# Optimization experiments

Measured on AMD Instinct MI355X. Metric: run time of the kernel, lower is better.

The kernel has to match this reference:

```python
import jax, jax.numpy as jnp
import numpy as np

DIM = 256
HEADS = 8
SEQ = 4096
SCALE = DIM ** -0.5  # note: original scales by full dim, not head dim


def setup_inputs() -> dict:
    key = jax.random.key(0)
    ks = jax.random.split(key, 5)
    x = jax.random.normal(ks[0], (SEQ, DIM), dtype=jnp.float32)
    w_qkv = jax.random.normal(ks[1], (DIM, 3 * DIM), dtype=jnp.float32) * (DIM ** -0.5)
    b_qkv = jnp.zeros((3 * DIM,), dtype=jnp.float32)
    w_out = jax.random.normal(ks[2], (DIM, DIM), dtype=jnp.float32) * (DIM ** -0.5)
    b_out = jnp.zeros((DIM,), dtype=jnp.float32)
    return {"x": x, "w_qkv": w_qkv, "b_qkv": b_qkv, "w_out": w_out, "b_out": b_out}


def reference(x, w_qkv, b_qkv, w_out, b_out):
    n, dim = x.shape
    h = HEADS
    d = dim // h
    qkv = x @ w_qkv + b_qkv                      # [n, 3*dim]
    q, k, v = jnp.split(qkv, 3, axis=-1)         # each [n, dim]
    # 'n (h d) -> h n d'
    q = q.reshape(n, h, d).transpose(1, 0, 2)
    k = k.reshape(n, h, d).transpose(1, 0, 2)
    v = v.reshape(n, h, d).transpose(1, 0, 2)
    dots = jnp.einsum('hid,hjd->hij', q, k) * SCALE  # [h, n, n]
    attn = jax.nn.softmax(dots, axis=-1)
    out = jnp.einsum('hij,hjd->hid', attn, v)        # [h, n, d]
    out = out.transpose(1, 0, 2).reshape(n, dim)     # 'h n d -> n (h d)'
    return out @ w_out + b_out                       # [n, dim]
```

## Files before the change

### kernel.cpp

```cpp
#include <hip/hip_runtime.h>
#include <stdint.h>

#define SEQ   4096
#define DIM   256
#define HDIM  32
#define HEADS 8
#define W3    768
#define LOG2E 1.4426950408889634f

typedef float  f32x4  __attribute__((ext_vector_type(4)));
typedef float  fl4    __attribute__((ext_vector_type(4)));
typedef short  bf16x8 __attribute__((ext_vector_type(8)));
typedef short  bf16x4 __attribute__((ext_vector_type(4)));

static __device__ __forceinline__ f32x4 MFMA_PV(bf16x4 a, bf16x4 b, f32x4 c) {
#if defined(__HIP_DEVICE_COMPILE__)
# if __has_builtin(__builtin_amdgcn_mfma_f32_16x16x16_bf16)
    return __builtin_amdgcn_mfma_f32_16x16x16_bf16(a, b, c, 0, 0, 0);
# elif __has_builtin(__builtin_amdgcn_mfma_f32_16x16x16bf16_1k)
    return __builtin_amdgcn_mfma_f32_16x16x16bf16_1k(a, b, c, 0, 0, 0);
# else
    f32x4 d;
    asm volatile("v_mfma_f32_16x16x16_bf16 %0, %1, %2, %3"
                 : "=v"(d) : "v"(a), "v"(b), "v"(c));
    return d;
# endif
#else
    (void)a; (void)b;
    return c;
#endif
}

__device__ __forceinline__ unsigned short f2bf(float f) {
    union { __bf16 h; unsigned short u; } v;
    v.h = (__bf16)f;
    return v.u;
}
__device__ __forceinline__ short f2bf_s(float f) {
    union { __bf16 h; short s; } v;
    v.h = (__bf16)f;
    return v.s;
}

__global__ __launch_bounds__(256) void prep_kernel(
    const float* __restrict__ x, const float* __restrict__ wqkv,
    const float* __restrict__ wout,
    unsigned short* __restrict__ xb,
    unsigned short* __restrict__ wt,
    unsigned short* __restrict__ wot)
{
    __shared__ float lds[64][65];
    const int b   = blockIdx.x;
    const int tid = threadIdx.x;
    if (b < 64) {
        const float* src;
        unsigned short* dst;
        int N, i0, j0;
        if (b < 48) {
            src = wqkv; dst = wt; N = W3;
            i0 = (b & 3) * 64; j0 = (b >> 2) * 64;
        } else {
            int bb = b - 48;
            src = wout; dst = wot; N = DIM;
            i0 = (bb & 3) * 64; j0 = (bb >> 2) * 64;
        }
        const int c = tid & 63, grp = tid >> 6;
        #pragma unroll
        for (int k = 0; k < 16; ++k) {
            int r = grp * 16 + k;
            lds[r][c] = src[(size_t)(i0 + r) * N + j0 + c];
        }
        __syncthreads();
        #pragma unroll
        for (int k = 0; k < 16; ++k) {
            int cc = grp * 16 + k;
            dst[(size_t)(j0 + cc) * DIM + i0 + c] = f2bf(lds[c][cc]);
        }
    } else {
        const fl4* __restrict__ x4 = (const fl4*)x;
        const int total4 = SEQ * DIM / 4;
        for (int i = (b - 64) * 256 + tid; i < total4; i += 64 * 256) {
            fl4 v = x4[i];
            ushort4 o;
            o.x = f2bf(v[0]); o.y = f2bf(v[1]);
            o.z = f2bf(v[2]); o.w = f2bf(v[3]);
            *reinterpret_cast<ushort4*>(xb + (size_t)i * 4) = o;
        }
    }
}

__global__ __launch_bounds__(256) void qkv_gemm(
    const unsigned short* __restrict__ xb,
    const unsigned short* __restrict__ wt,
    const float* __restrict__ bqkv,
    unsigned short* __restrict__ Qb,
    unsigned short* __restrict__ Kb,
    unsigned short* __restrict__ Vb)
{
    const int wid  = threadIdx.x >> 6;
    const int lane = threadIdx.x & 63;
    const int g    = lane >> 4, li = lane & 15;
    const int row0 = blockIdx.x * 64 + wid * 16;
    const int col0 = blockIdx.y * 64;

    f32x4 acc[4];
    #pragma unroll
    for (int c = 0; c < 4; ++c)
        acc[c] = (f32x4){0.f, 0.f, 0.f, 0.f};

    #pragma unroll
    for (int ks = 0; ks < DIM; ks += 32) {
        bf16x8 a = *(const bf16x8*)(xb + (size_t)(row0 + li) * DIM + ks + g * 8);
        bf16x8 b[4];
        #pragma unroll
        for (int c = 0; c < 4; ++c)
            b[c] = *(const bf16x8*)(wt + (size_t)(col0 + 16 * c + li) * DIM + ks + g * 8);
        #pragma unroll
        for (int c = 0; c < 4; ++c)
            acc[c] = __builtin_amdgcn_mfma_f32_16x16x32_bf16(a, b[c], acc[c], 0, 0, 0);
    }

    #pragma unroll
    for (int c = 0; c < 4; ++c)
        #pragma unroll
        for (int r = 0; r < 4; ++r) {
            int row = row0 + g * 4 + r;
            int col = col0 + 16 * c + li;
            float v = acc[c][r] + bqkv[col];
            int sec = col >> 8;
            int cc  = col & 255;
            int hh  = cc >> 5, dd = cc & 31;
            if (sec == 0)
                Qb[((size_t)hh * SEQ + row) * HDIM + dd] = f2bf(v * (0.0625f * LOG2E));
            else if (sec == 1)
                Kb[((size_t)hh * SEQ + row) * HDIM + dd] = f2bf(v);
            else
                Vb[(size_t)hh * SEQ * HDIM + ((size_t)(row >> 4) * HDIM + dd) * 16 + (row & 15)] = f2bf(v);
        }
}

__global__ __launch_bounds__(256) void attn_kernel(
    const unsigned short* __restrict__ Qb,
    const unsigned short* __restrict__ Kb,
    const unsigned short* __restrict__ Vb,
    float* __restrict__ Opart,
    float* __restrict__ Lp,
    int nc)
{
    const int wid  = threadIdx.x >> 6;
    const int lane = threadIdx.x & 63;
    const int g    = lane >> 4, li = lane & 15;
    const int head = blockIdx.y;
    const int chunk = blockIdx.z;
    const int r0   = blockIdx.x * 128 + wid * 32;
    const int span = SEQ / nc;
    const int jb0  = chunk * span;
    const int ntile = span / 64;

    const unsigned short* Qh = Qb + (size_t)head * SEQ * HDIM;
    const unsigned short* kp = Kb + (size_t)head * SEQ * HDIM + (size_t)jb0 * HDIM
                             + (size_t)li * HDIM + g * 8;
    const unsigned short* vp = Vb + (size_t)head * SEQ * HDIM + (size_t)jb0 * HDIM
                             + (size_t)li * 16 + 4 * g;

    bf16x8 aq[2];
    #pragma unroll
    for (int t = 0; t < 2; ++t)
        aq[t] = *(const bf16x8*)(Qh + (size_t)(r0 + 16 * t + li) * HDIM + g * 8);

    f32x4 o[2][2];
    #pragma unroll
    for (int t = 0; t < 2; ++t)
        #pragma unroll
        for (int nt = 0; nt < 2; ++nt)
            o[t][nt] = (f32x4){0.f, 0.f, 0.f, 0.f};
    float lacc[2] = {0.f, 0.f};

    const f32x4 zero4 = (f32x4){0.f, 0.f, 0.f, 0.f};

#define LOADK(DST, P) do {                                                    \
    _Pragma("unroll")                                                         \
    for (int c_ = 0; c_ < 4; ++c_)                                            \
        DST[c_] = *(const bf16x8*)((P) + c_ * (16 * HDIM));                   \
} while (0)

#define LOADV(DST, P) do {                                                    \
    _Pragma("unroll")                                                         \
    for (int c_ = 0; c_ < 4; ++c_)                                            \
        _Pragma("unroll")                                                     \
        for (int nt_ = 0; nt_ < 2; ++nt_)                                     \
            DST[c_][nt_] = *(const bf16x4*)((P) + c_ * (16 * HDIM) + nt_ * 256); \
} while (0)

#define TILE(BK, BV) do {                                                     \
    bf16x4 pa_[2][4];                                                         \
    _Pragma("unroll")                                                         \
    for (int t_ = 0; t_ < 2; ++t_) {                                          \
        f32x4 s_[4];                                                          \
        __builtin_amdgcn_s_setprio(1);                                        \
        _Pragma("unroll")                                                     \
        for (int c_ = 0; c_ < 4; ++c_)                                        \
            s_[c_] = __builtin_amdgcn_mfma_f32_16x16x32_bf16(BK[c_], aq[t_], zero4, 0, 0, 0); \
        __builtin_amdgcn_s_setprio(0);                                        \
        _Pragma("unroll")                                                     \
        for (int c_ = 0; c_ < 4; ++c_) {                                      \
            float p0_ = __builtin_amdgcn_exp2f(s_[c_][0]);                    \
            float p1_ = __builtin_amdgcn_exp2f(s_[c_][1]);                    \
            float p2_ = __builtin_amdgcn_exp2f(s_[c_][2]);                    \
            float p3_ = __builtin_amdgcn_exp2f(s_[c_][3]);                    \
            lacc[t_] += (p0_ + p1_) + (p2_ + p3_);                            \
            bf16x4 f_;                                                        \
            f_[0] = f2bf_s(p0_); f_[1] = f2bf_s(p1_);                         \
            f_[2] = f2bf_s(p2_); f_[3] = f2bf_s(p3_);                         \
            pa_[t_][c_] = f_;                                                 \
        }                                                                     \
    }                                                                         \
    __builtin_amdgcn_s_setprio(1);                                            \
    _Pragma("unroll")                                                         \
    for (int c_ = 0; c_ < 4; ++c_)                                            \
        _Pragma("unroll")                                                     \
        for (int t_ = 0; t_ < 2; ++t_)                                        \
            _Pragma("unroll")                                                 \
            for (int nt_ = 0; nt_ < 2; ++nt_)                                 \
                o[t_][nt_] = MFMA_PV(pa_[t_][c_], BV[c_][nt_], o[t_][nt_]);   \
    __builtin_amdgcn_s_setprio(0);                                            \
} while (0)

    bf16x8 bkA[4], bkB[4];
    bf16x4 bvA[4][2], bvB[4][2];
    LOADK(bkA, kp);
    LOADV(bvA, vp);
    for (int i = 0; i < ntile - 2; i += 2) {
        LOADK(bkB, kp + 2048);
        LOADV(bvB, vp + 2048);
        TILE(bkA, bvA);
        LOADK(bkA, kp + 4096);
        LOADV(bvA, vp + 4096);
        TILE(bkB, bvB);
        kp += 4096; vp += 4096;
    }
    LOADK(bkB, kp + 2048);
    LOADV(bvB, vp + 2048);
    TILE(bkA, bvA);
    TILE(bkB, bvB);
#undef LOADK
#undef LOADV
#undef TILE

    #pragma unroll
    for (int t = 0; t < 2; ++t) {
        float L = lacc[t];
        L += __shfl_xor(L, 16);
        L += __shfl_xor(L, 32);
        lacc[t] = L;
    }

    float* Oc = Opart + (size_t)chunk * SEQ * DIM;
    #pragma unroll
    for (int t = 0; t < 2; ++t)
        #pragma unroll
        for (int nt = 0; nt < 2; ++nt)
            #pragma unroll
            for (int r = 0; r < 4; ++r) {
                int row = r0 + 16 * t + g * 4 + r;
                int col = head * HDIM + 16 * nt + li;
                Oc[(size_t)row * DIM + col] = o[t][nt][r];
            }
    if (lane < 16) {
        #pragma unroll
        for (int t = 0; t < 2; ++t) {
            int row = r0 + 16 * t + lane;
            Lp[((size_t)chunk * HEADS + head) * SEQ + row] = lacc[t];
        }
    }
}

__global__ __launch_bounds__(256) void combine_kernel(
    const float* __restrict__ Opart, const float* __restrict__ Lp,
    unsigned short* __restrict__ AO, int nc)
{
    int idx = blockIdx.x * 256 + threadIdx.x;
    int row = idx >> 7;
    int cp  = (idx & 127) << 1;
    int head = cp >> 5;
    float L = 0.f, a0 = 0.f, a1 = 0.f;
    for (int i = 0; i < nc; ++i) {
        L += Lp[((size_t)i * HEADS + head) * SEQ + row];
        const float* op = Opart + (size_t)i * SEQ * DIM + (size_t)row * DIM + cp;
        a0 += op[0];
        a1 += op[1];
    }
    float inv = 1.f / L;
    uint32_t pk = (uint32_t)f2bf(a0 * inv) | ((uint32_t)f2bf(a1 * inv) << 16);
    *reinterpret_cast<uint32_t*>(AO + (size_t)row * DIM + cp) = pk;
}

__global__ __launch_bounds__(256) void out_gemm(
    const unsigned short* __restrict__ AO,
    const unsigned short* __restrict__ wot,
    const float* __restrict__ bout,
    float* __restrict__ out)
{
    const int wid  = threadIdx.x >> 6;
    const int lane = threadIdx.x & 63;
    const int g    = lane >> 4, li = lane & 15;
    const int row0 = blockIdx.x * 64 + wid * 16;
    const int col0 = blockIdx.y * 64;

    f32x4 acc[4];
    #pragma unroll
    for (int c = 0; c < 4; ++c)
        acc[c] = (f32x4){0.f, 0.f, 0.f, 0.f};

    #pragma unroll
    for (int ks = 0; ks < DIM; ks += 32) {
        bf16x8 a = *(const bf16x8*)(AO + (size_t)(row0 + li) * DIM + ks + g * 8);
        bf16x8 b[4];
        #pragma unroll
        for (int c = 0; c < 4; ++c)
            b[c] = *(const bf16x8*)(wot + (size_t)(col0 + 16 * c + li) * DIM + ks + g * 8);
        #pragma unroll
        for (int c = 0; c < 4; ++c)
            acc[c] = __builtin_amdgcn_mfma_f32_16x16x32_bf16(a, b[c], acc[c], 0, 0, 0);
    }

    #pragma unroll
    for (int c = 0; c < 4; ++c)
        #pragma unroll
        for (int r = 0; r < 4; ++r) {
            int row = row0 + g * 4 + r;
            int col = col0 + 16 * c + li;
            out[(size_t)row * DIM + col] = acc[c][r] + bout[col];
        }
}

extern "C" void kernel_launch(void* const* d_in, const int* in_sizes, int n_in,
                              void* d_out, int out_size, void* d_ws, size_t ws_size,
                              hipStream_t stream)
{
    const float* x    = (const float*)d_in[0];
    const float* wqkv = (const float*)d_in[1];
    const float* bqkv = (const float*)d_in[2];
    const float* wout = (const float*)d_in[3];
    const float* bout = (const float*)d_in[4];
    float* out = (float*)d_out;

    char* ws = (char*)d_ws;
    const size_t OFF_XB  = 0;
    const size_t OFF_WT  = 2097152;
    const size_t OFF_WOT = 2490368;
    const size_t OFF_QB  = 2621440;
    const size_t OFF_KB  = 4718592;
    const size_t OFF_VT  = 6815744;
    const size_t OFF_AO  = 8912896;
    const size_t OFF_OP  = 11010048;
    const size_t OP_CH   = (size_t)SEQ * DIM * 4;
    const size_t LP_CH   = (size_t)HEADS * SEQ * 4;

    int nc = 8;
    while (nc > 1 && OFF_OP + (size_t)nc * (OP_CH + LP_CH) > ws_size) nc >>= 1;
    if (OFF_OP + (size_t)nc * (OP_CH + LP_CH) > ws_size) return;

    unsigned short* xb  = (unsigned short*)(ws + OFF_XB);
    unsigned short* wt  = (unsigned short*)(ws + OFF_WT);
    unsigned short* wot = (unsigned short*)(ws + OFF_WOT);
    unsigned short* Qb  = (unsigned short*)(ws + OFF_QB);
    unsigned short* Kb  = (unsigned short*)(ws + OFF_KB);
    unsigned short* Vb  = (unsigned short*)(ws + OFF_VT);
    unsigned short* AO  = (unsigned short*)(ws + OFF_AO);
    float* Opart = (float*)(ws + OFF_OP);
    float* Lp    = (float*)(ws + OFF_OP + (size_t)nc * OP_CH);

    hipLaunchKernelGGL(prep_kernel, dim3(128), dim3(256), 0, stream,
                       x, wqkv, wout, xb, wt, wot);
    hipLaunchKernelGGL(qkv_gemm, dim3(64, 12), dim3(256), 0, stream,
                       xb, wt, bqkv, Qb, Kb, Vb);
    hipLaunchKernelGGL(attn_kernel, dim3(SEQ / 128, HEADS, nc), dim3(256), 0, stream,
                       Qb, Kb, Vb, Opart, Lp, nc);
    hipLaunchKernelGGL(combine_kernel, dim3(SEQ * DIM / 512), dim3(256), 0, stream,
                       Opart, Lp, AO, nc);
    hipLaunchKernelGGL(out_gemm, dim3(SEQ / 64, DIM / 64), dim3(256), 0, stream,
                       AO, wot, bout, out);
}
```

Measured before the change: 80.08 us.

## Split KV span across wave pairs in-block, reduce via LDS, halve chunk count

Each attention block now covers 64 query rows. Its four waves form two pairs that process the two halves of the chunk's key span, and the partial outputs and row sums are merged through shared memory before a single write. The number of global KV chunks drops from 8 to 4, which halves the Opart/Lp partial traffic and the work in the combine kernel. The combine kernel is vectorised to float4 loads and 4-wide bf16 stores. V loads move inside the tile macro and the s_setprio hints are removed, which changes latency hiding and register pressure; the extra __syncthreads and LDS round trip add some cost.

```diff
diff --git a/kernel.cpp b/kernel.cpp
--- a/kernel.cpp
+++ b/kernel.cpp
@@ -147,15 +147,20 @@
     float* __restrict__ Lp,
     int nc)
 {
+    __shared__ float obuf[2][16 * 64];
+    __shared__ float lbuf[2][2 * 64];
     const int wid  = threadIdx.x >> 6;
     const int lane = threadIdx.x & 63;
     const int g    = lane >> 4, li = lane & 15;
     const int head = blockIdx.y;
     const int chunk = blockIdx.z;
-    const int r0   = blockIdx.x * 128 + wid * 32;
-    const int span = SEQ / nc;
-    const int jb0  = chunk * span;
-    const int ntile = span / 64;
+    const int qs   = wid & 1;
+    const int half = wid >> 1;
+    const int r0   = blockIdx.x * 64 + qs * 32;
+    const int span  = SEQ / nc;
+    const int wspan = span >> 1;
+    const int jb0   = chunk * span + half * wspan;
+    const int ntile = wspan / 64;
 
     const unsigned short* Qh = Qb + (size_t)head * SEQ * HDIM;
     const unsigned short* kp = Kb + (size_t)head * SEQ * HDIM + (size_t)jb0 * HDIM
@@ -184,24 +189,20 @@
         DST[c_] = *(const bf16x8*)((P) + c_ * (16 * HDIM));                   \
 } while (0)
 
-#define LOADV(DST, P) do {                                                    \
+#define TILE(BK, VP) do {                                                     \
+    bf16x4 bv_[4][2];                                                         \
     _Pragma("unroll")                                                         \
     for (int c_ = 0; c_ < 4; ++c_)                                            \
         _Pragma("unroll")                                                     \
         for (int nt_ = 0; nt_ < 2; ++nt_)                                     \
-            DST[c_][nt_] = *(const bf16x4*)((P) + c_ * (16 * HDIM) + nt_ * 256); \
-} while (0)
-
-#define TILE(BK, BV) do {                                                     \
+            bv_[c_][nt_] = *(const bf16x4*)((VP) + c_ * (16 * HDIM) + nt_ * 256); \
     bf16x4 pa_[2][4];                                                         \
     _Pragma("unroll")                                                         \
     for (int t_ = 0; t_ < 2; ++t_) {                                          \
         f32x4 s_[4];                                                          \
-        __builtin_amdgcn_s_setprio(1);                                        \
         _Pragma("unroll")                                                     \
         for (int c_ = 0; c_ < 4; ++c_)                                        \
             s_[c_] = __builtin_amdgcn_mfma_f32_16x16x32_bf16(BK[c_], aq[t_], zero4, 0, 0, 0); \
-        __builtin_amdgcn_s_setprio(0);                                        \
         _Pragma("unroll")                                                     \
         for (int c_ = 0; c_ < 4; ++c_) {                                      \
             float p0_ = __builtin_amdgcn_exp2f(s_[c_][0]);                    \
@@ -215,37 +216,55 @@
             pa_[t_][c_] = f_;                                                 \
         }                                                                     \
     }                                                                         \
-    __builtin_amdgcn_s_setprio(1);                                            \
     _Pragma("unroll")                                                         \
     for (int c_ = 0; c_ < 4; ++c_)                                            \
         _Pragma("unroll")                                                     \
         for (int t_ = 0; t_ < 2; ++t_)                                        \
             _Pragma("unroll")                                                 \
             for (int nt_ = 0; nt_ < 2; ++nt_)                                 \
-                o[t_][nt_] = MFMA_PV(pa_[t_][c_], BV[c_][nt_], o[t_][nt_]);   \
-    __builtin_amdgcn_s_setprio(0);                                            \
+                o[t_][nt_] = MFMA_PV(pa_[t_][c_], bv_[c_][nt_], o[t_][nt_]);  \
 } while (0)
 
     bf16x8 bkA[4], bkB[4];
-    bf16x4 bvA[4][2], bvB[4][2];
     LOADK(bkA, kp);
-    LOADV(bvA, vp);
     for (int i = 0; i < ntile - 2; i += 2) {
         LOADK(bkB, kp + 2048);
-        LOADV(bvB, vp + 2048);
-        TILE(bkA, bvA);
+        TILE(bkA, vp);
         LOADK(bkA, kp + 4096);
-        LOADV(bvA, vp + 4096);
-        TILE(bkB, bvB);
+        TILE(bkB, vp + 2048);
         kp += 4096; vp += 4096;
     }
     LOADK(bkB, kp + 2048);
-    LOADV(bvB, vp + 2048);
-    TILE(bkA, bvA);
-    TILE(bkB, bvB);
+    TILE(bkA, vp);
+    TILE(bkB, vp + 2048);
 #undef LOADK
-#undef LOADV
 #undef TILE
+
+    if (half == 1) {
+        #pragma unroll
+        for (int t = 0; t < 2; ++t)
+            #pragma unroll
+            for (int nt = 0; nt < 2; ++nt)
+                #pragma unroll
+                for (int r = 0; r < 4; ++r)
+                    obuf[qs][((t * 2 + nt) * 4 + r) * 64 + lane] = o[t][nt][r];
+        #pragma unroll
+        for (int t = 0; t < 2; ++t)
+            lbuf[qs][t * 64 + lane] = lacc[t];
+    }
+    __syncthreads();
+    if (half == 1) return;
+
+    #pragma unroll
+    for (int t = 0; t < 2; ++t)
+        #pragma unroll
+        for (int nt = 0; nt < 2; ++nt)
+            #pragma unroll
+            for (int r = 0; r < 4; ++r)
+                o[t][nt][r] += obuf[qs][((t * 2 + nt) * 4 + r) * 64 + lane];
+    #pragma unroll
+    for (int t = 0; t < 2; ++t)
+        lacc[t] += lbuf[qs][t * 64 + lane];
 
     #pragma unroll
     for (int t = 0; t < 2; ++t) {
@@ -280,19 +299,20 @@
     unsigned short* __restrict__ AO, int nc)
 {
     int idx = blockIdx.x * 256 + threadIdx.x;
-    int row = idx >> 7;
-    int cp  = (idx & 127) << 1;
+    int row = idx >> 6;
+    int cp  = (idx & 63) << 2;
     int head = cp >> 5;
-    float L = 0.f, a0 = 0.f, a1 = 0.f;
+    float L = 0.f;
+    fl4 a = (fl4){0.f, 0.f, 0.f, 0.f};
     for (int i = 0; i < nc; ++i) {
         L += Lp[((size_t)i * HEADS + head) * SEQ + row];
-        const float* op = Opart + (size_t)i * SEQ * DIM + (size_t)row * DIM + cp;
-        a0 += op[0];
-        a1 += op[1];
+        a += *(const fl4*)(Opart + (size_t)i * SEQ * DIM + (size_t)row * DIM + cp);
     }
     float inv = 1.f / L;
-    uint32_t pk = (uint32_t)f2bf(a0 * inv) | ((uint32_t)f2bf(a1 * inv) << 16);
-    *reinterpret_cast<uint32_t*>(AO + (size_t)row * DIM + cp) = pk;
+    ushort4 pk;
+    pk.x = f2bf(a[0] * inv); pk.y = f2bf(a[1] * inv);
+    pk.z = f2bf(a[2] * inv); pk.w = f2bf(a[3] * inv);
+    *reinterpret_cast<ushort4*>(AO + (size_t)row * DIM + cp) = pk;
 }
 
 __global__ __launch_bounds__(256) void out_gemm(
@@ -357,7 +377,7 @@
     const size_t OP_CH   = (size_t)SEQ * DIM * 4;
     const size_t LP_CH   = (size_t)HEADS * SEQ * 4;
 
-    int nc = 8;
+    int nc = 4;
     while (nc > 1 && OFF_OP + (size_t)nc * (OP_CH + LP_CH) > ws_size) nc >>= 1;
     if (OFF_OP + (size_t)nc * (OP_CH + LP_CH) > ws_size) return;
 
@@ -375,9 +395,9 @@
                        x, wqkv, wout, xb, wt, wot);
     hipLaunchKernelGGL(qkv_gemm, dim3(64, 12), dim3(256), 0, stream,
                        xb, wt, bqkv, Qb, Kb, Vb);
-    hipLaunchKernelGGL(attn_kernel, dim3(SEQ / 128, HEADS, nc), dim3(256), 0, stream,
+    hipLaunchKernelGGL(attn_kernel, dim3(SEQ / 64, HEADS, nc), dim3(256), 0, stream,
                        Qb, Kb, Vb, Opart, Lp, nc);
-    hipLaunchKernelGGL(combine_kernel, dim3(SEQ * DIM / 512), dim3(256), 0, stream,
+    hipLaunchKernelGGL(combine_kernel, dim3(SEQ * DIM / 1024), dim3(256), 0, stream,
                        Opart, Lp, AO, nc);
     hipLaunchKernelGGL(out_gemm, dim3(SEQ / 64, DIM / 64), dim3(256), 0, stream,
                        AO, wot, bout, out);
```

New measurement: 75.77 us. 1.06x faster.
